# Kernel optimization log

Measured on AMD Instinct MI355X. Metric: run time of the kernel, lower is better.

The kernel has to match this reference:

```python
import jax, jax.numpy as jnp
import numpy as np

B, S, D_MODEL, N_HEADS = 2, 256, 512, 8
HEAD_DIM = D_MODEL // N_HEADS  # 64; k.size(-1) used for scaling


def setup_inputs() -> dict:
    key = jax.random.key(0)
    ks = jax.random.split(key, 11)
    sd = 1.0 / np.sqrt(D_MODEL)
    sf = 1.0 / np.sqrt(N_HEADS * D_MODEL)
    return {
        "Q": jax.random.normal(ks[0], (B, S, D_MODEL), jnp.float32),
        "K": jax.random.normal(ks[1], (B, S, D_MODEL), jnp.float32),
        "V": jax.random.normal(ks[2], (B, S, D_MODEL), jnp.float32),
        "Wq": jax.random.normal(ks[3], (D_MODEL, D_MODEL * N_HEADS), jnp.float32) * sd,
        "bq": jax.random.normal(ks[4], (D_MODEL * N_HEADS,), jnp.float32) * sd,
        "Wk": jax.random.normal(ks[5], (D_MODEL, D_MODEL * N_HEADS), jnp.float32) * sd,
        "bk": jax.random.normal(ks[6], (D_MODEL * N_HEADS,), jnp.float32) * sd,
        "Wv": jax.random.normal(ks[7], (D_MODEL, D_MODEL * N_HEADS), jnp.float32) * sd,
        "bv": jax.random.normal(ks[8], (D_MODEL * N_HEADS,), jnp.float32) * sd,
        "Wf": jax.random.normal(ks[9], (N_HEADS * D_MODEL, D_MODEL), jnp.float32) * sf,
        "bf": jax.random.normal(ks[10], (D_MODEL,), jnp.float32) * sf,
    }


def _split_heads(x):
    # Faithful to torch: view(B, -1, n_heads, d_model//n_heads).transpose(1, 2).
    # x: (B, S, D_MODEL*N_HEADS) -> (B, N_HEADS, S*N_HEADS, HEAD_DIM)
    b = x.shape[0]
    return jnp.transpose(x.reshape(b, -1, N_HEADS, HEAD_DIM), (0, 2, 1, 3))


def reference(Q, K, V, Wq, bq, Wk, bk, Wv, bv, Wf, bf):
    q = _split_heads(Q @ Wq + bq)  # (B, H, S*H, Dh)
    k = _split_heads(K @ Wk + bk)
    v = _split_heads(V @ Wv + bv)
    scale = 1.0 / jnp.sqrt(jnp.float32(HEAD_DIM))
    scores = jnp.einsum("bhqd,bhkd->bhqk", q, k) * scale  # (B, H, S*H, S*H)
    weights = jax.nn.softmax(scores, axis=-1)
    ctx = jnp.einsum("bhqk,bhkd->bhqd", weights, v)  # (B, H, S*H, Dh)
    # transpose(1,2).view(B, -1, n_heads*d_model) -> (B, S, N_HEADS*D_MODEL)
    ctx = jnp.transpose(ctx, (0, 2, 1, 3)).reshape(Q.shape[0], -1, N_HEADS * D_MODEL)
    return ctx @ Wf + bf  # (B, S, D_MODEL)
```

## Files before the change

### kernel.cpp

```cpp
#include <hip/hip_runtime.h>
#include <hip/hip_bf16.h>


typedef __attribute__((ext_vector_type(4))) float f32x4;
typedef __attribute__((ext_vector_type(8))) short short8;
typedef __attribute__((ext_vector_type(4))) short short4v;
typedef __attribute__((ext_vector_type(4))) unsigned int u32x4;

#define SEQ 2048
#define DH 64
#define BH 16
#define ROWS 512
#define DM 512
#define NQ 4096
#define KSPLIT 8

static __device__ __forceinline__ unsigned short f2bf(float f) {
    return __builtin_bit_cast(unsigned short, __float2bfloat16(f));
}
static __device__ __forceinline__ short4v pk4(float a, float b, float c, float d) {
    return short4v{(short)f2bf(a), (short)f2bf(b), (short)f2bf(c), (short)f2bf(d)};
}
static __device__ __forceinline__ unsigned cvt_pk_bf16(float lo, float hi) {
    unsigned r;
    asm("v_cvt_pk_bf16_f32 %0, %1, %2" : "=v"(r) : "v"(lo), "v"(hi));
    return r;
}

__global__ __launch_bounds__(256) void qkv_proj_kernel(
    const float* __restrict__ Q, const float* __restrict__ K, const float* __restrict__ V,
    const float* __restrict__ Wq, const float* __restrict__ bq,
    const float* __restrict__ Wk, const float* __restrict__ bk,
    const float* __restrict__ Wv, const float* __restrict__ bv,
    unsigned short* __restrict__ q_bf, unsigned short* __restrict__ k_bf,
    unsigned short* __restrict__ vT_bf)
{
    const int mat = blockIdx.z;
    const float* X    = (mat == 0) ? Q  : (mat == 1) ? K  : V;
    const float* W    = (mat == 0) ? Wq : (mat == 1) ? Wk : Wv;
    const float* bias = (mat == 0) ? bq : (mat == 1) ? bk : bv;

    const int n0 = blockIdx.x * 64;
    const int m0 = blockIdx.y * 64;
    const int tid = threadIdx.x;
    const int w = tid >> 6, l = tid & 63;
    const int lr = l & 15, lg = l >> 4;

    __shared__ unsigned short a_lds[64][72];
    __shared__ unsigned short wt_lds[64 * 72];

    const int xr0 = tid >> 4, xc4 = (tid & 15) * 4;
    const int wn = tid & 63, wkseg = tid >> 6;
    const int wxr = (wn >> 3) & 7;

    f32x4 acc[4];
#pragma unroll
    for (int ct = 0; ct < 4; ++ct) acc[ct] = f32x4{0.f, 0.f, 0.f, 0.f};

    float4 rx[4];
    float rwv[16];

#pragma unroll
    for (int i = 0; i < 4; ++i)
        rx[i] = *reinterpret_cast<const float4*>(X + (m0 + i * 16 + xr0) * DM + xc4);
#pragma unroll
    for (int j = 0; j < 16; ++j)
        rwv[j] = W[(size_t)(wkseg * 16 + j) * NQ + n0 + wn];

    for (int t = 0; t < 8; ++t) {
#pragma unroll
        for (int i = 0; i < 4; ++i)
            *reinterpret_cast<short4v*>(&a_lds[i * 16 + xr0][xc4]) =
                pk4(rx[i].x, rx[i].y, rx[i].z, rx[i].w);
#pragma unroll
        for (int j4 = 0; j4 < 4; ++j4) {
            int kb = wkseg * 2 + (j4 >> 1);
            int off = wn * 72 + ((kb ^ wxr) << 3) + (j4 & 1) * 4;
            *reinterpret_cast<short4v*>(&wt_lds[off]) =
                pk4(rwv[j4 * 4 + 0], rwv[j4 * 4 + 1], rwv[j4 * 4 + 2], rwv[j4 * 4 + 3]);
        }
        __syncthreads();

        if (t < 7) {
            int k0 = (t + 1) * 64;
#pragma unroll
            for (int i = 0; i < 4; ++i)
                rx[i] = *reinterpret_cast<const float4*>(X + (m0 + i * 16 + xr0) * DM + k0 + xc4);
#pragma unroll
            for (int j = 0; j < 16; ++j)
                rwv[j] = W[(size_t)(k0 + wkseg * 16 + j) * NQ + n0 + wn];
        }

#pragma unroll
        for (int ks = 0; ks < 2; ++ks) {
            short8 a = *reinterpret_cast<const short8*>(&a_lds[w * 16 + lr][ks * 32 + lg * 8]);
#pragma unroll
            for (int ct = 0; ct < 4; ++ct) {
                int row = ct * 16 + lr;
                int kb = ks * 4 + lg;
                short8 b = *reinterpret_cast<const short8*>(
                    &wt_lds[row * 72 + ((kb ^ ((row >> 3) & 7)) << 3)]);
                acc[ct] = __builtin_amdgcn_mfma_f32_16x16x32_bf16(a, b, acc[ct], 0, 0, 0);
            }
        }
        __syncthreads();
    }

#pragma unroll
    for (int ct = 0; ct < 4; ++ct) {
        int c = n0 + ct * 16 + lr;
        float bv_ = bias[c];
        int h = (c >> 6) & 7, d = c & 63, c1 = c >> 9;
#pragma unroll
        for (int r = 0; r < 4; ++r) {
            int row = m0 + w * 16 + lg * 4 + r;
            int b = row >> 8, s = row & 255;
            int n = s * 8 + c1;
            unsigned short bfv = f2bf(acc[ct][r] + bv_);
            if (mat == 0)      q_bf[((b * 8 + h) * SEQ + n) * DH + d] = bfv;
            else if (mat == 1) k_bf[((b * 8 + h) * SEQ + n) * DH + d] = bfv;
            else               vT_bf[((b * 8 + h) * DH + d) * SEQ + n] = bfv;
        }
    }
}

__global__ __launch_bounds__(512, 4) void attn_split_kernel(
    const unsigned short* __restrict__ q_bf,
    const unsigned short* __restrict__ k_bf,
    const unsigned short* __restrict__ vT_bf,
    float* __restrict__ po,
    float* __restrict__ pl)
{
    const int bh = blockIdx.y;
    const int z = blockIdx.z;
    const int n0 = blockIdx.x * 64;
    const int tid = threadIdx.x;
    const int w = tid >> 6, l = tid & 63;
    const int wq = w & 3, sub = w >> 2;
    const int lr = l & 15, lg = l >> 4;
    const int gtid = tid & 255;

    po += (size_t)z * BH * SEQ * 64;
    pl += (size_t)z * BH * SEQ;

    const unsigned short* qb = q_bf + (size_t)bh * SEQ * DH;
    const unsigned short* kb = k_bf + (size_t)bh * SEQ * DH;
    const unsigned short* vb = vT_bf + (size_t)bh * DH * SEQ;

    __shared__ __align__(16) unsigned short kvl[4][64][72];
    __shared__ float l_red[4][16];

    const int qrow = n0 + wq * 16 + lr;
    short8 aq[2];
    aq[0] = *reinterpret_cast<const short8*>(qb + qrow * DH + lg * 8);
    aq[1] = *reinterpret_cast<const short8*>(qb + qrow * DH + 32 + lg * 8);

    f32x4 o[4];
#pragma unroll
    for (int i = 0; i < 4; ++i) o[i] = f32x4{0.f, 0.f, 0.f, 0.f};
    float l_part = 0.f;

    const int srow = gtid >> 3, sc8 = (gtid & 7) * 8;
    const int kbase0 = z * (SEQ / 2) + sub * (SEQ / 4);

    short8 rk[2], rv[2];
#pragma unroll
    for (int i = 0; i < 2; ++i) {
        int row = srow + i * 32;
        rk[i] = *reinterpret_cast<const short8*>(kb + (kbase0 + row) * DH + sc8);
        rv[i] = *reinterpret_cast<const short8*>(vb + row * SEQ + kbase0 + sc8);
    }

    const bool lowc  = (lg < 2);
    const bool sendR = (lg == 0) || (lg == 3);
    const bool oddlg = (lg & 1);

    for (int kt = 0; kt < SEQ / 4 / 64; ++kt) {
#pragma unroll
        for (int i = 0; i < 2; ++i) {
            *reinterpret_cast<short8*>(&kvl[sub][srow + i * 32][sc8]) = rk[i];
            *reinterpret_cast<short8*>(&kvl[2 + sub][srow + i * 32][sc8]) = rv[i];
        }
        __syncthreads();

        if (kt < SEQ / 4 / 64 - 1) {
            int kb0 = kbase0 + (kt + 1) * 64;
#pragma unroll
            for (int i = 0; i < 2; ++i) {
                int row = srow + i * 32;
                rk[i] = *reinterpret_cast<const short8*>(kb + (kb0 + row) * DH + sc8);
                rv[i] = *reinterpret_cast<const short8*>(vb + row * SEQ + kb0 + sc8);
            }
        }

        f32x4 s[4];
#pragma unroll
        for (int ct = 0; ct < 4; ++ct) s[ct] = f32x4{0.f, 0.f, 0.f, 0.f};
#pragma unroll
        for (int ks = 0; ks < 2; ++ks) {
#pragma unroll
            for (int ct = 0; ct < 4; ++ct) {
                short8 kfrag = *reinterpret_cast<const short8*>(&kvl[sub][ct * 16 + lr][ks * 32 + lg * 8]);
                s[ct] = __builtin_amdgcn_mfma_f32_16x16x32_bf16(kfrag, aq[ks], s[ct], 0, 0, 0);
            }
        }

        float rs_t = 0.f;
#pragma unroll
        for (int ct = 0; ct < 4; ++ct)
#pragma unroll
            for (int r = 0; r < 4; ++r) {
                float pv = exp2f(s[ct][r] * 0.18033688011112042f);
                s[ct][r] = pv;
                rs_t += pv;
            }
        l_part += rs_t;

        unsigned Wp[8];
#pragma unroll
        for (int c = 0; c < 4; ++c) {
            Wp[c * 2 + 0] = cvt_pk_bf16(s[c][0], s[c][1]);
            Wp[c * 2 + 1] = cvt_pk_bf16(s[c][2], s[c][3]);
        }

        unsigned keepA[4], r1r[4];
#pragma unroll
        for (int a = 0; a < 2; ++a)
#pragma unroll
            for (int hh = 0; hh < 2; ++hh) {
                int i = a * 2 + hh;
                unsigned snd = lowc ? Wp[(2 * a + 1) * 2 + hh] : Wp[(2 * a) * 2 + hh];
                keepA[i]     = lowc ? Wp[(2 * a) * 2 + hh]     : Wp[(2 * a + 1) * 2 + hh];
                r1r[i] = (unsigned)__shfl_xor((int)snd, 32);
            }
        unsigned r2k[4], r2r[4];
#pragma unroll
        for (int i = 0; i < 4; ++i) {
            unsigned snd = sendR ? r1r[i] : keepA[i];
            r2k[i]       = sendR ? keepA[i] : r1r[i];
            r2r[i] = (unsigned)__shfl_xor((int)snd, 16);
        }

        u32x4 pbu[2];
#pragma unroll
        for (int ks = 0; ks < 2; ++ks) {
            unsigned g0a = oddlg ? r2r[2 * ks + 0] : r2k[2 * ks + 0];
            unsigned g0b = oddlg ? r2r[2 * ks + 1] : r2k[2 * ks + 1];
            unsigned g1a = oddlg ? r2k[2 * ks + 0] : r2r[2 * ks + 0];
            unsigned g1b = oddlg ? r2k[2 * ks + 1] : r2r[2 * ks + 1];
            pbu[ks] = u32x4{g0a, g0b, g1a, g1b};
        }

#pragma unroll
        for (int ks = 0; ks < 2; ++ks) {
            short8 pfrag = __builtin_bit_cast(short8, pbu[ks]);
#pragma unroll
            for (int dt = 0; dt < 4; ++dt) {
                short8 vfrag = *reinterpret_cast<const short8*>(&kvl[2 + sub][dt * 16 + lr][ks * 32 + lg * 8]);
                o[dt] = __builtin_amdgcn_mfma_f32_16x16x32_bf16(vfrag, pfrag, o[dt], 0, 0, 0);
            }
        }
        __syncthreads();
    }

    float rs = l_part;
    rs += __shfl_xor(rs, 16);
    rs += __shfl_xor(rs, 32);

    float* o_red = (float*)&kvl[0][0][0];
    const int orow = (wq * 16 + lr) * 72;
    if (sub == 1) {
#pragma unroll
        for (int dt = 0; dt < 4; ++dt)
            *reinterpret_cast<f32x4*>(&o_red[orow + dt * 16 + lg * 4]) = o[dt];
        if (lg == 0) l_red[wq][lr] = rs;
    }
    __syncthreads();
    if (sub == 0) {
        float l_blk = rs + l_red[wq][lr];
        int n = n0 + wq * 16 + lr;
        size_t rbase = ((size_t)bh * SEQ + n) * 64;
#pragma unroll
        for (int dt = 0; dt < 4; ++dt) {
            f32x4 oo = *reinterpret_cast<f32x4*>(&o_red[orow + dt * 16 + lg * 4]);
            oo += o[dt];
            *reinterpret_cast<f32x4*>(po + rbase + dt * 16 + lg * 4) = oo;
        }
        if (lg == 0) pl[bh * SEQ + n] = l_blk;
    }
}

__global__ __launch_bounds__(256) void attn_merge_kernel(
    const float* __restrict__ po,
    const float* __restrict__ pl,
    unsigned short* __restrict__ ctx_bf)
{
    int t = blockIdx.x * 256 + threadIdx.x;
    int cg = t & 15, r = t >> 4;
    const size_t Z = (size_t)BH * SEQ * 64;
    float inv = 1.f / (pl[r] + pl[BH * SEQ + r]);
    f32x4 a = *reinterpret_cast<const f32x4*>(po + (size_t)r * 64 + cg * 4);
    f32x4 b = *reinterpret_cast<const f32x4*>(po + Z + (size_t)r * 64 + cg * 4);
    a = (a + b) * inv;
    int bh = r >> 11, n = r & (SEQ - 1);
    int bb = bh >> 3, h = bh & 7, sp = n >> 3;
    int cbase = (n & 7) * 512 + h * 64;
    *reinterpret_cast<short4v*>(ctx_bf + (size_t)(bb * 256 + sp) * NQ + cbase + cg * 4) =
        pk4(a[0], a[1], a[2], a[3]);
}

__global__ __launch_bounds__(512, 4) void attn_kernel(
    const unsigned short* __restrict__ q_bf,
    const unsigned short* __restrict__ k_bf,
    const unsigned short* __restrict__ vT_bf,
    unsigned short* __restrict__ ctx_bf)
{
    const int bh = blockIdx.y;
    const int b = bh >> 3, h = bh & 7;
    const int n0 = blockIdx.x * 64;
    const int tid = threadIdx.x;
    const int w = tid >> 6, l = tid & 63;
    const int wq = w & 3, half = w >> 2;
    const int lr = l & 15, lg = l >> 4;
    const int gtid = tid & 255;

    const unsigned short* qb = q_bf + (size_t)bh * SEQ * DH;
    const unsigned short* kb = k_bf + (size_t)bh * SEQ * DH;
    const unsigned short* vb = vT_bf + (size_t)bh * DH * SEQ;

    __shared__ __align__(16) unsigned short kvl[4][64][72];
    __shared__ float l_red[4][16];

    const int qrow = n0 + wq * 16 + lr;
    short8 aq[2];
    aq[0] = *reinterpret_cast<const short8*>(qb + qrow * DH + lg * 8);
    aq[1] = *reinterpret_cast<const short8*>(qb + qrow * DH + 32 + lg * 8);

    f32x4 o[4];
#pragma unroll
    for (int i = 0; i < 4; ++i) o[i] = f32x4{0.f, 0.f, 0.f, 0.f};
    float l_part = 0.f;

    const int srow = gtid >> 3, sc8 = (gtid & 7) * 8;
    const int kbase0 = half * (SEQ / 2);

    short8 rk[2], rv[2];
#pragma unroll
    for (int i = 0; i < 2; ++i) {
        int row = srow + i * 32;
        rk[i] = *reinterpret_cast<const short8*>(kb + (kbase0 + row) * DH + sc8);
        rv[i] = *reinterpret_cast<const short8*>(vb + row * SEQ + kbase0 + sc8);
    }

    const bool lowc  = (lg < 2);
    const bool sendR = (lg == 0) || (lg == 3);
    const bool oddlg = (lg & 1);

    for (int kt = 0; kt < SEQ / 2 / 64; ++kt) {
#pragma unroll
        for (int i = 0; i < 2; ++i) {
            *reinterpret_cast<short8*>(&kvl[half & 1][srow + i * 32][sc8]) = rk[i];
            *reinterpret_cast<short8*>(&kvl[2 + (half & 1)][srow + i * 32][sc8]) = rv[i];
        }
        __syncthreads();

        if (kt < SEQ / 2 / 64 - 1) {
            int kb0 = kbase0 + (kt + 1) * 64;
#pragma unroll
            for (int i = 0; i < 2; ++i) {
                int row = srow + i * 32;
                rk[i] = *reinterpret_cast<const short8*>(kb + (kb0 + row) * DH + sc8);
                rv[i] = *reinterpret_cast<const short8*>(vb + row * SEQ + kb0 + sc8);
            }
        }

        f32x4 s[4];
#pragma unroll
        for (int ct = 0; ct < 4; ++ct) s[ct] = f32x4{0.f, 0.f, 0.f, 0.f};
#pragma unroll
        for (int ks = 0; ks < 2; ++ks) {
#pragma unroll
            for (int ct = 0; ct < 4; ++ct) {
                short8 kfrag = *reinterpret_cast<const short8*>(&kvl[half][ct * 16 + lr][ks * 32 + lg * 8]);
                s[ct] = __builtin_amdgcn_mfma_f32_16x16x32_bf16(kfrag, aq[ks], s[ct], 0, 0, 0);
            }
        }

        float rs_t = 0.f;
#pragma unroll
        for (int ct = 0; ct < 4; ++ct)
#pragma unroll
            for (int r = 0; r < 4; ++r) {
                float pv = exp2f(s[ct][r] * 0.18033688011112042f);
                s[ct][r] = pv;
                rs_t += pv;
            }
        l_part += rs_t;

        unsigned Wp[8];
#pragma unroll
        for (int c = 0; c < 4; ++c) {
            Wp[c * 2 + 0] = cvt_pk_bf16(s[c][0], s[c][1]);
            Wp[c * 2 + 1] = cvt_pk_bf16(s[c][2], s[c][3]);
        }

        unsigned keepA[4], r1r[4];
#pragma unroll
        for (int a = 0; a < 2; ++a)
#pragma unroll
            for (int hh = 0; hh < 2; ++hh) {
                int i = a * 2 + hh;
                unsigned snd = lowc ? Wp[(2 * a + 1) * 2 + hh] : Wp[(2 * a) * 2 + hh];
                keepA[i]     = lowc ? Wp[(2 * a) * 2 + hh]     : Wp[(2 * a + 1) * 2 + hh];
                r1r[i] = (unsigned)__shfl_xor((int)snd, 32);
            }
        unsigned r2k[4], r2r[4];
#pragma unroll
        for (int i = 0; i < 4; ++i) {
            unsigned snd = sendR ? r1r[i] : keepA[i];
            r2k[i]       = sendR ? keepA[i] : r1r[i];
            r2r[i] = (unsigned)__shfl_xor((int)snd, 16);
        }

        u32x4 pbu[2];
#pragma unroll
        for (int ks = 0; ks < 2; ++ks) {
            unsigned g0a = oddlg ? r2r[2 * ks + 0] : r2k[2 * ks + 0];
            unsigned g0b = oddlg ? r2r[2 * ks + 1] : r2k[2 * ks + 1];
            unsigned g1a = oddlg ? r2k[2 * ks + 0] : r2r[2 * ks + 0];
            unsigned g1b = oddlg ? r2k[2 * ks + 1] : r2r[2 * ks + 1];
            pbu[ks] = u32x4{g0a, g0b, g1a, g1b};
        }

#pragma unroll
        for (int ks = 0; ks < 2; ++ks) {
            short8 pfrag = __builtin_bit_cast(short8, pbu[ks]);
#pragma unroll
            for (int dt = 0; dt < 4; ++dt) {
                short8 vfrag = *reinterpret_cast<const short8*>(&kvl[2 + half][dt * 16 + lr][ks * 32 + lg * 8]);
                o[dt] = __builtin_amdgcn_mfma_f32_16x16x32_bf16(vfrag, pfrag, o[dt], 0, 0, 0);
            }
        }
        __syncthreads();
    }

    float rs = l_part;
    rs += __shfl_xor(rs, 16);
    rs += __shfl_xor(rs, 32);

    float* o_red = (float*)&kvl[0][0][0];
    const int orow = (wq * 16 + lr) * 72;
    if (half == 1) {
#pragma unroll
        for (int dt = 0; dt < 4; ++dt)
            *reinterpret_cast<f32x4*>(&o_red[orow + dt * 16 + lg * 4]) = o[dt];
        if (lg == 0) l_red[wq][lr] = rs;
    }
    __syncthreads();
    if (half == 0) {
        float inv = 1.f / (rs + l_red[wq][lr]);
        int n = n0 + wq * 16 + lr;
        int sp = n >> 3;
        int cbase = (n & 7) * 512 + h * 64;
        unsigned short* dst = ctx_bf + (size_t)(b * 256 + sp) * NQ + cbase;
#pragma unroll
        for (int dt = 0; dt < 4; ++dt) {
            f32x4 oo = *reinterpret_cast<f32x4*>(&o_red[orow + dt * 16 + lg * 4]);
            oo = (o[dt] + oo) * inv;
            *reinterpret_cast<short4v*>(dst + dt * 16 + lg * 4) = pk4(oo[0], oo[1], oo[2], oo[3]);
        }
    }
}

__global__ __launch_bounds__(256) void out_proj_splitk_kernel(
    const unsigned short* __restrict__ ctx_bf,
    const float* __restrict__ Wf,
    float* __restrict__ part)
{
    const int n0 = blockIdx.x * 64;
    const int m0 = blockIdx.y * 64;
    const int ksplit = blockIdx.z;
    const int kbase = ksplit * (NQ / KSPLIT);
    const int tid = threadIdx.x;
    const int w = tid >> 6, l = tid & 63;
    const int lr = l & 15, lg = l >> 4;

    __shared__ unsigned short a_lds[64][72];
    __shared__ unsigned short wt_lds[64 * 72];

    const int arow0 = tid >> 3, ac8 = (tid & 7) * 8;
    const int wn = tid & 63, wkseg = tid >> 6;
    const int wxr = (wn >> 3) & 7;

    f32x4 acc[4];
#pragma unroll
    for (int ct = 0; ct < 4; ++ct) acc[ct] = f32x4{0.f, 0.f, 0.f, 0.f};

    short8 ra[2];
    float rwv[16];

    {
#pragma unroll
        for (int i = 0; i < 2; ++i)
            ra[i] = *reinterpret_cast<const short8*>(
                ctx_bf + (size_t)(m0 + arow0 + i * 32) * NQ + kbase + ac8);
#pragma unroll
        for (int j = 0; j < 16; ++j)
            rwv[j] = Wf[(size_t)(kbase + wkseg * 16 + j) * DM + n0 + wn];
    }

    for (int t = 0; t < 8; ++t) {
#pragma unroll
        for (int i = 0; i < 2; ++i)
            *reinterpret_cast<short8*>(&a_lds[arow0 + i * 32][ac8]) = ra[i];
#pragma unroll
        for (int j4 = 0; j4 < 4; ++j4) {
            int kb = wkseg * 2 + (j4 >> 1);
            int off = wn * 72 + ((kb ^ wxr) << 3) + (j4 & 1) * 4;
            *reinterpret_cast<short4v*>(&wt_lds[off]) =
                pk4(rwv[j4 * 4 + 0], rwv[j4 * 4 + 1], rwv[j4 * 4 + 2], rwv[j4 * 4 + 3]);
        }
        __syncthreads();

        if (t < 7) {
            int k0 = kbase + (t + 1) * 64;
#pragma unroll
            for (int i = 0; i < 2; ++i)
                ra[i] = *reinterpret_cast<const short8*>(
                    ctx_bf + (size_t)(m0 + arow0 + i * 32) * NQ + k0 + ac8);
#pragma unroll
            for (int j = 0; j < 16; ++j)
                rwv[j] = Wf[(size_t)(k0 + wkseg * 16 + j) * DM + n0 + wn];
        }

#pragma unroll
        for (int ks = 0; ks < 2; ++ks) {
            short8 a = *reinterpret_cast<const short8*>(&a_lds[w * 16 + lr][ks * 32 + lg * 8]);
#pragma unroll
            for (int ct = 0; ct < 4; ++ct) {
                int row = ct * 16 + lr;
                int kb = ks * 4 + lg;
                short8 b = *reinterpret_cast<const short8*>(
                    &wt_lds[row * 72 + ((kb ^ ((row >> 3) & 7)) << 3)]);
                acc[ct] = __builtin_amdgcn_mfma_f32_16x16x32_bf16(a, b, acc[ct], 0, 0, 0);
            }
        }
        __syncthreads();
    }

    float* pbase = part + (size_t)ksplit * ROWS * DM;
#pragma unroll
    for (int ct = 0; ct < 4; ++ct) {
        int c = n0 + ct * 16 + lr;
#pragma unroll
        for (int r = 0; r < 4; ++r) {
            int row = m0 + w * 16 + lg * 4 + r;
            pbase[(size_t)row * DM + c] = acc[ct][r];
        }
    }
}

__global__ __launch_bounds__(256) void out_reduce_kernel(
    const float* __restrict__ part, const float* __restrict__ bf_,
    float* __restrict__ out)
{
    int i4 = blockIdx.x * 256 + threadIdx.x;
    int e = i4 * 4;
    float4 acc = *reinterpret_cast<const float4*>(bf_ + (e & (DM - 1)));
#pragma unroll
    for (int ks = 0; ks < KSPLIT; ++ks) {
        float4 p = *reinterpret_cast<const float4*>(part + (size_t)ks * ROWS * DM + e);
        acc.x += p.x; acc.y += p.y; acc.z += p.z; acc.w += p.w;
    }
    *reinterpret_cast<float4*>(out + e) = acc;
}

extern "C" void kernel_launch(void* const* d_in, const int* in_sizes, int n_in,
                              void* d_out, int out_size, void* d_ws, size_t ws_size,
                              hipStream_t stream) {
    const float* Q  = (const float*)d_in[0];
    const float* K  = (const float*)d_in[1];
    const float* V  = (const float*)d_in[2];
    const float* Wq = (const float*)d_in[3];
    const float* bq = (const float*)d_in[4];
    const float* Wk = (const float*)d_in[5];
    const float* bk = (const float*)d_in[6];
    const float* Wv = (const float*)d_in[7];
    const float* bv = (const float*)d_in[8];
    const float* Wf = (const float*)d_in[9];
    const float* bf = (const float*)d_in[10];
    float* out = (float*)d_out;

    unsigned short* q_bf  = (unsigned short*)d_ws;
    unsigned short* k_bf  = q_bf + (size_t)BH * SEQ * DH;
    unsigned short* vT_bf = k_bf + (size_t)BH * SEQ * DH;
    unsigned short* ctx_bf = vT_bf + (size_t)BH * SEQ * DH;
    float* part = (float*)d_ws;

    const size_t base16 = (size_t)BH * SEQ * DH * 3 * 2 + (size_t)ROWS * NQ * 2;
    float* po = (float*)((char*)d_ws + base16);
    float* pl = po + (size_t)2 * BH * SEQ * 64;
    const size_t required = base16 + (size_t)2 * BH * SEQ * 64 * 4 + (size_t)2 * BH * SEQ * 4;

    qkv_proj_kernel<<<dim3(NQ / 64, ROWS / 64, 3), 256, 0, stream>>>(
        Q, K, V, Wq, bq, Wk, bk, Wv, bv, q_bf, k_bf, vT_bf);

    if (ws_size >= required) {
        attn_split_kernel<<<dim3(SEQ / 64, BH, 2), 512, 0, stream>>>(
            q_bf, k_bf, vT_bf, po, pl);
        attn_merge_kernel<<<dim3(BH * SEQ * 16 / 256), 256, 0, stream>>>(po, pl, ctx_bf);
    } else {
        attn_kernel<<<dim3(SEQ / 64, BH), 512, 0, stream>>>(q_bf, k_bf, vT_bf, ctx_bf);
    }

    out_proj_splitk_kernel<<<dim3(DM / 64, ROWS / 64, KSPLIT), 256, 0, stream>>>(
        ctx_bf, Wf, part);
    out_reduce_kernel<<<dim3(ROWS * DM / 4 / 256), 256, 0, stream>>>(part, bf, out);
}
```

Measured before the change: 93.14 us.

## Read K/V fragments directly from global memory in split attention, drop LDS staging

The split-attention kernel no longer stages K and V tiles through shared memory with barriers. Each of four waves now loads its MFMA fragments straight from global memory (relying on L1/L2 caching) and walks the full half of the key range. This also removes the intra-block two-way key split and its shared-memory reduction, halving the block size to 256 threads. It trades LDS traffic and syncs for redundant global/L2 loads and less parallelism per block, with no explicit prefetch.

```diff
diff --git a/kernel.cpp b/kernel.cpp
--- a/kernel.cpp
+++ b/kernel.cpp
@@ -124,7 +124,7 @@
     }
 }
 
-__global__ __launch_bounds__(512, 4) void attn_split_kernel(
+__global__ __launch_bounds__(256, 4) void attn_split_kernel(
     const unsigned short* __restrict__ q_bf,
     const unsigned short* __restrict__ k_bf,
     const unsigned short* __restrict__ vT_bf,
@@ -136,9 +136,7 @@
     const int n0 = blockIdx.x * 64;
     const int tid = threadIdx.x;
     const int w = tid >> 6, l = tid & 63;
-    const int wq = w & 3, sub = w >> 2;
     const int lr = l & 15, lg = l >> 4;
-    const int gtid = tid & 255;
 
     po += (size_t)z * BH * SEQ * 64;
     pl += (size_t)z * BH * SEQ;
@@ -147,10 +145,7 @@
     const unsigned short* kb = k_bf + (size_t)bh * SEQ * DH;
     const unsigned short* vb = vT_bf + (size_t)bh * DH * SEQ;
 
-    __shared__ __align__(16) unsigned short kvl[4][64][72];
-    __shared__ float l_red[4][16];
-
-    const int qrow = n0 + wq * 16 + lr;
+    const int qrow = n0 + w * 16 + lr;
     short8 aq[2];
     aq[0] = *reinterpret_cast<const short8*>(qb + qrow * DH + lg * 8);
     aq[1] = *reinterpret_cast<const short8*>(qb + qrow * DH + 32 + lg * 8);
@@ -160,38 +155,16 @@
     for (int i = 0; i < 4; ++i) o[i] = f32x4{0.f, 0.f, 0.f, 0.f};
     float l_part = 0.f;
 
-    const int srow = gtid >> 3, sc8 = (gtid & 7) * 8;
-    const int kbase0 = z * (SEQ / 2) + sub * (SEQ / 4);
-
-    short8 rk[2], rv[2];
-#pragma unroll
-    for (int i = 0; i < 2; ++i) {
-        int row = srow + i * 32;
-        rk[i] = *reinterpret_cast<const short8*>(kb + (kbase0 + row) * DH + sc8);
-        rv[i] = *reinterpret_cast<const short8*>(vb + row * SEQ + kbase0 + sc8);
-    }
+    const int kz = z * (SEQ / 2);
+    const unsigned short* kp = kb + (size_t)(kz + lr) * DH + lg * 8;
+    const unsigned short* vp = vb + (size_t)lr * SEQ + kz + lg * 8;
 
     const bool lowc  = (lg < 2);
     const bool sendR = (lg == 0) || (lg == 3);
     const bool oddlg = (lg & 1);
 
-    for (int kt = 0; kt < SEQ / 4 / 64; ++kt) {
-#pragma unroll
-        for (int i = 0; i < 2; ++i) {
-            *reinterpret_cast<short8*>(&kvl[sub][srow + i * 32][sc8]) = rk[i];
-            *reinterpret_cast<short8*>(&kvl[2 + sub][srow + i * 32][sc8]) = rv[i];
-        }
-        __syncthreads();
-
-        if (kt < SEQ / 4 / 64 - 1) {
-            int kb0 = kbase0 + (kt + 1) * 64;
-#pragma unroll
-            for (int i = 0; i < 2; ++i) {
-                int row = srow + i * 32;
-                rk[i] = *reinterpret_cast<const short8*>(kb + (kb0 + row) * DH + sc8);
-                rv[i] = *reinterpret_cast<const short8*>(vb + row * SEQ + kb0 + sc8);
-            }
-        }
+    for (int kt = 0; kt < SEQ / 2 / 64; ++kt) {
+        const unsigned short* kpt = kp + kt * 64 * DH;
 
         f32x4 s[4];
 #pragma unroll
@@ -200,7 +173,7 @@
         for (int ks = 0; ks < 2; ++ks) {
 #pragma unroll
             for (int ct = 0; ct < 4; ++ct) {
-                short8 kfrag = *reinterpret_cast<const short8*>(&kvl[sub][ct * 16 + lr][ks * 32 + lg * 8]);
+                short8 kfrag = *reinterpret_cast<const short8*>(kpt + ct * 16 * DH + ks * 32);
                 s[ct] = __builtin_amdgcn_mfma_f32_16x16x32_bf16(kfrag, aq[ks], s[ct], 0, 0, 0);
             }
         }
@@ -251,43 +224,28 @@
             pbu[ks] = u32x4{g0a, g0b, g1a, g1b};
         }
 
+        const unsigned short* vpt = vp + kt * 64;
 #pragma unroll
         for (int ks = 0; ks < 2; ++ks) {
             short8 pfrag = __builtin_bit_cast(short8, pbu[ks]);
 #pragma unroll
             for (int dt = 0; dt < 4; ++dt) {
-                short8 vfrag = *reinterpret_cast<const short8*>(&kvl[2 + sub][dt * 16 + lr][ks * 32 + lg * 8]);
+                short8 vfrag = *reinterpret_cast<const short8*>(vpt + dt * 16 * SEQ + ks * 32);
                 o[dt] = __builtin_amdgcn_mfma_f32_16x16x32_bf16(vfrag, pfrag, o[dt], 0, 0, 0);
             }
         }
-        __syncthreads();
     }
 
     float rs = l_part;
     rs += __shfl_xor(rs, 16);
     rs += __shfl_xor(rs, 32);
 
-    float* o_red = (float*)&kvl[0][0][0];
-    const int orow = (wq * 16 + lr) * 72;
-    if (sub == 1) {
-#pragma unroll
-        for (int dt = 0; dt < 4; ++dt)
-            *reinterpret_cast<f32x4*>(&o_red[orow + dt * 16 + lg * 4]) = o[dt];
-        if (lg == 0) l_red[wq][lr] = rs;
-    }
-    __syncthreads();
-    if (sub == 0) {
-        float l_blk = rs + l_red[wq][lr];
-        int n = n0 + wq * 16 + lr;
-        size_t rbase = ((size_t)bh * SEQ + n) * 64;
-#pragma unroll
-        for (int dt = 0; dt < 4; ++dt) {
-            f32x4 oo = *reinterpret_cast<f32x4*>(&o_red[orow + dt * 16 + lg * 4]);
-            oo += o[dt];
-            *reinterpret_cast<f32x4*>(po + rbase + dt * 16 + lg * 4) = oo;
-        }
-        if (lg == 0) pl[bh * SEQ + n] = l_blk;
-    }
+    int n = n0 + w * 16 + lr;
+    size_t rbase = ((size_t)bh * SEQ + n) * 64;
+#pragma unroll
+    for (int dt = 0; dt < 4; ++dt)
+        *reinterpret_cast<f32x4*>(po + rbase + dt * 16 + lg * 4) = o[dt];
+    if (lg == 0) pl[bh * SEQ + n] = rs;
 }
 
 __global__ __launch_bounds__(256) void attn_merge_kernel(
@@ -359,8 +317,8 @@
     for (int kt = 0; kt < SEQ / 2 / 64; ++kt) {
 #pragma unroll
         for (int i = 0; i < 2; ++i) {
-            *reinterpret_cast<short8*>(&kvl[half & 1][srow + i * 32][sc8]) = rk[i];
-            *reinterpret_cast<short8*>(&kvl[2 + (half & 1)][srow + i * 32][sc8]) = rv[i];
+            *reinterpret_cast<short8*>(&kvl[half][srow + i * 32][sc8]) = rk[i];
+            *reinterpret_cast<short8*>(&kvl[2 + half][srow + i * 32][sc8]) = rv[i];
         }
         __syncthreads();
 
@@ -606,7 +564,7 @@
         Q, K, V, Wq, bq, Wk, bk, Wv, bv, q_bf, k_bf, vT_bf);
 
     if (ws_size >= required) {
-        attn_split_kernel<<<dim3(SEQ / 64, BH, 2), 512, 0, stream>>>(
+        attn_split_kernel<<<dim3(SEQ / 64, BH, 2), 256, 0, stream>>>(
             q_bf, k_bf, vT_bf, po, pl);
         attn_merge_kernel<<<dim3(BH * SEQ * 16 / 256), 256, 0, stream>>>(po, pl, ctx_bf);
     } else {
```

Result: slower. 166.9 us (+79.2%).
